# Performance work log

Hardware: AMD Instinct MI355X
Metric: run time of the kernel (lower is better)

Reference implementation:

```python
import jax, jax.numpy as jnp
import numpy as np

N_U = 8192  # users (rows of adj)
N_I = 8192  # items (cols of adj)
D_IN = 2048
D_H = 2048


def setup_inputs() -> dict:
    key = jax.random.key(0)
    k1, k2, k3, k4, k5 = jax.random.split(key, 5)
    input = jax.random.normal(k1, (N_U + N_I, D_IN), dtype=jnp.float32)
    adj = jax.random.uniform(k2, (N_U, N_I), dtype=jnp.float32)
    degree = jax.random.uniform(k3, (N_U + N_I,), dtype=jnp.float32)
    # Linear params (torch Linear: y = x @ W.T + b), xavier-normal-ish init
    W = jax.random.normal(k4, (D_H, D_IN), dtype=jnp.float32) * (2.0 / (D_IN + D_H)) ** 0.5
    b = jax.random.normal(k5, (D_H,), dtype=jnp.float32) * 0.01
    return {"input": input, "adj": adj, "degree": degree, "W": W, "b": b}


def reference(input, adj, degree, W, b):
    # Original builds block adjacency B = [[0, A], [A^T, 0]], then
    # output = diag(degree) @ B @ (dropout(input) @ W^T + b).
    # dropout p=0 (eval) -> identity. We avoid materializing B: the block
    # structure means user rows aggregate item supports and vice versa.
    n_u = adj.shape[0]
    support = input @ W.T + b                      # [N_u+N_i, D_h]
    sup_u, sup_i = support[:n_u], support[n_u:]
    out_u = degree[:n_u, None] * (adj @ sup_i)     # [N_u, D_h]
    out_i = degree[n_u:, None] * (adj.T @ sup_u)   # [N_i, D_h]
    return jnp.concatenate([out_u, out_i], axis=0)
```

## Files before the change

### kernel.cpp

```cpp
#include <hip/hip_runtime.h>
#include <hip/hip_bf16.h>


typedef __bf16 bf16;
typedef bf16 bf16x4 __attribute__((ext_vector_type(4)));
typedef bf16 bf16x8 __attribute__((ext_vector_type(8)));
typedef float f32x4 __attribute__((ext_vector_type(4)));

#define AS1 __attribute__((address_space(1)))
#define AS3 __attribute__((address_space(3)))

__global__ __launch_bounds__(256) void k_cvt(const float* __restrict__ src,
                                             bf16* __restrict__ dst) {
  long i = ((long)blockIdx.x * 256 + threadIdx.x) * 4;
  float4 v = *(const float4*)(src + i);
  bf16x4 o;
  o.x = (bf16)v.x; o.y = (bf16)v.y; o.z = (bf16)v.z; o.w = (bf16)v.w;
  *(bf16x4*)(dst + i) = o;
}

__global__ __launch_bounds__(256) void k_transpose_cvt(const float* __restrict__ src,
                                                       bf16* __restrict__ dst, int n) {
  __shared__ float tile[64][65];
  const int bx = blockIdx.x * 64;
  const int by = blockIdx.y * 64;
  const int tx = threadIdx.x & 15, ty = threadIdx.x >> 4;
#pragma unroll
  for (int p = 0; p < 4; ++p) {
    float4 v = *(const float4*)(src + (long)(by + p * 16 + ty) * n + bx + tx * 4);
    tile[p * 16 + ty][tx * 4 + 0] = v.x;
    tile[p * 16 + ty][tx * 4 + 1] = v.y;
    tile[p * 16 + ty][tx * 4 + 2] = v.z;
    tile[p * 16 + ty][tx * 4 + 3] = v.w;
  }
  __syncthreads();
#pragma unroll
  for (int p = 0; p < 4; ++p) {
    bf16x4 o;
    o.x = (bf16)tile[tx * 4 + 0][p * 16 + ty];
    o.y = (bf16)tile[tx * 4 + 1][p * 16 + ty];
    o.z = (bf16)tile[tx * 4 + 2][p * 16 + ty];
    o.w = (bf16)tile[tx * 4 + 3][p * 16 + ty];
    *(bf16x4*)(dst + (long)(bx + p * 16 + ty) * n + by + tx * 4) = o;
  }
}

template <bool OUT_BF16>
__global__ __launch_bounds__(256) void k_gemm_nt(
    const bf16* __restrict__ A, const bf16* __restrict__ B, void* __restrict__ Cout,
    int K, int lda, int ldb, int ldc,
    const float* __restrict__ rowscale, const float* __restrict__ rowbias) {
  constexpr int BK = 64;
  __shared__ __align__(16) bf16 As[128 * BK];
  __shared__ __align__(16) bf16 Bs[128 * BK];
  const int tid = threadIdx.x;
  const int wave = tid >> 6, lane = tid & 63;
  const int quad = lane >> 4, l16 = lane & 15;
  const int bm = blockIdx.y * 128, bn = blockIdx.x * 128;
  const bf16* Ab = A + (long)bm * lda;
  const bf16* Bb = B + (long)bn * ldb;
  f32x4 acc[4][4] = {};
  const int mrow = (wave & 1) * 64 + l16;
  const int ncol = (wave >> 1) * 64 + l16;
  const int xm = l16 & 7;

  for (int k0 = 0; k0 < K; k0 += BK) {
    __syncthreads();
#pragma unroll
    for (int it = 0; it < 4; ++it) {
      const int c = it * 256 + tid;
      const int row = c >> 3;
      const int kc = ((c & 7) ^ (row & 7)) * 8;
      __builtin_amdgcn_global_load_lds((AS1 void*)(Ab + row * lda + k0 + kc),
                                       (AS3 void*)(As + c * 8), 16, 0, 0);
      __builtin_amdgcn_global_load_lds((AS1 void*)(Bb + row * ldb + k0 + kc),
                                       (AS3 void*)(Bs + c * 8), 16, 0, 0);
    }
    __syncthreads();
#pragma unroll
    for (int ks = 0; ks < 2; ++ks) {
      const int jl = ks * 4 + quad;
      bf16x8 af[4], bfr[4];
#pragma unroll
      for (int i = 0; i < 4; ++i)
        af[i] = *(const bf16x8*)(As + (mrow + i * 16) * BK + ((jl ^ xm) << 3));
#pragma unroll
      for (int j = 0; j < 4; ++j)
        bfr[j] = *(const bf16x8*)(Bs + (ncol + j * 16) * BK + ((jl ^ xm) << 3));
#pragma unroll
      for (int i = 0; i < 4; ++i)
#pragma unroll
        for (int j = 0; j < 4; ++j)
          acc[i][j] = __builtin_amdgcn_mfma_f32_16x16x32_bf16(af[i], bfr[j], acc[i][j], 0, 0, 0);
    }
  }

#pragma unroll
  for (int i = 0; i < 4; ++i) {
    const int r0 = bm + (wave & 1) * 64 + i * 16 + quad * 4;
    float sc[4], bi[4];
#pragma unroll
    for (int r = 0; r < 4; ++r) {
      sc[r] = rowscale ? rowscale[r0 + r] : 1.0f;
      bi[r] = rowbias ? rowbias[r0 + r] : 0.0f;
    }
#pragma unroll
    for (int j = 0; j < 4; ++j) {
      const int col = bn + (wave >> 1) * 64 + j * 16 + l16;
#pragma unroll
      for (int r = 0; r < 4; ++r) {
        float v = acc[i][j][r] * sc[r] + bi[r];
        long idx = (long)(r0 + r) * ldc + col;
        if (OUT_BF16) ((bf16*)Cout)[idx] = (bf16)v;
        else          ((float*)Cout)[idx] = v;
      }
    }
  }
}

extern "C" void kernel_launch(void* const* d_in, const int* in_sizes, int n_in,
                              void* d_out, int out_size, void* d_ws, size_t ws_size,
                              hipStream_t stream) {
  const float* input  = (const float*)d_in[0];
  const float* adj    = (const float*)d_in[1];
  const float* degree = (const float*)d_in[2];
  const float* W      = (const float*)d_in[3];
  const float* b      = (const float*)d_in[4];
  float* out = (float*)d_out;

  char* ws = (char*)d_ws;
  bf16* supT   = (bf16*)(ws);
  bf16* in_bf  = (bf16*)(ws + (64ULL  << 20));
  bf16* W_bf   = (bf16*)(ws + (128ULL << 20));
  bf16* adj_bf = (bf16*)(ws + (64ULL  << 20));
  bf16* adjT   = (bf16*)(ws + (192ULL << 20));

  k_cvt<<<(16384 * 2048 / 4) / 256, 256, 0, stream>>>(input, in_bf);
  k_cvt<<<(2048 * 2048 / 4) / 256, 256, 0, stream>>>(W, W_bf);

  k_gemm_nt<true><<<dim3(16384 / 128, 2048 / 128), 256, 0, stream>>>(
      W_bf, in_bf, supT, 2048, 2048, 2048, 16384, nullptr, b);

  k_cvt<<<(8192 * 8192 / 4) / 256, 256, 0, stream>>>(adj, adj_bf);
  k_transpose_cvt<<<dim3(128, 128), 256, 0, stream>>>(adj, adjT, 8192);

  k_gemm_nt<false><<<dim3(2048 / 128, 8192 / 128), 256, 0, stream>>>(
      adj_bf, supT + 8192, out, 8192, 8192, 16384, 2048, degree, nullptr);

  k_gemm_nt<false><<<dim3(2048 / 128, 8192 / 128), 256, 0, stream>>>(
      adjT, supT, out + 8192LL * 2048, 8192, 8192, 16384, 2048, degree + 8192, nullptr);
}
```

Baseline: 1.423 ms.

## Fuse adj conversion passes, merge big GEMMs, add XCD-aware block swizzle

The separate adj bf16 cast and transpose-cast kernels become one kernel that reads adj once and writes both the row-major and transposed bf16 copies, which removes a full 256MB fp32 read. The two adjacency GEMMs are merged into a single launch using blockIdx.z, which removes a launch and tail gap. A block-index remap spreads contiguous row tiles across the 8 XCDs so tiles sharing A rows land on the same XCD's L2. The remap assumes grid.y is divisible by 8, and the merged kernel hard-codes the problem shapes.

New measurement: 1.458 ms. 1.02x slower.

```diff
diff --git a/kernel.cpp b/kernel.cpp
--- a/kernel.cpp
+++ b/kernel.cpp
@@ -19,15 +19,20 @@
   *(bf16x4*)(dst + i) = o;
 }
 
-__global__ __launch_bounds__(256) void k_transpose_cvt(const float* __restrict__ src,
-                                                       bf16* __restrict__ dst, int n) {
+__global__ __launch_bounds__(256) void k_adj_cvt_both(const float* __restrict__ src,
+                                                      bf16* __restrict__ dstS,
+                                                      bf16* __restrict__ dstT, int n) {
   __shared__ float tile[64][65];
   const int bx = blockIdx.x * 64;
   const int by = blockIdx.y * 64;
   const int tx = threadIdx.x & 15, ty = threadIdx.x >> 4;
 #pragma unroll
   for (int p = 0; p < 4; ++p) {
-    float4 v = *(const float4*)(src + (long)(by + p * 16 + ty) * n + bx + tx * 4);
+    const int row = by + p * 16 + ty;
+    float4 v = *(const float4*)(src + (long)row * n + bx + tx * 4);
+    bf16x4 s;
+    s.x = (bf16)v.x; s.y = (bf16)v.y; s.z = (bf16)v.z; s.w = (bf16)v.w;
+    *(bf16x4*)(dstS + (long)row * n + bx + tx * 4) = s;
     tile[p * 16 + ty][tx * 4 + 0] = v.x;
     tile[p * 16 + ty][tx * 4 + 1] = v.y;
     tile[p * 16 + ty][tx * 4 + 2] = v.z;
@@ -41,14 +46,22 @@
     o.y = (bf16)tile[tx * 4 + 1][p * 16 + ty];
     o.z = (bf16)tile[tx * 4 + 2][p * 16 + ty];
     o.w = (bf16)tile[tx * 4 + 3][p * 16 + ty];
-    *(bf16x4*)(dst + (long)(bx + p * 16 + ty) * n + by + tx * 4) = o;
+    *(bf16x4*)(dstT + (long)(bx + p * 16 + ty) * n + by + tx * 4) = o;
   }
 }
 
+__device__ inline void swizzle_xy(int nx, int ny, int& bxn, int& byn) {
+  const int id = blockIdx.y * nx + blockIdx.x;
+  const int xcd = id & 7;
+  const int slot = id >> 3;
+  bxn = slot % nx;
+  byn = xcd * (ny >> 3) + slot / nx;
+}
+
 template <bool OUT_BF16>
-__global__ __launch_bounds__(256) void k_gemm_nt(
+__device__ inline void gemm_nt_body(
     const bf16* __restrict__ A, const bf16* __restrict__ B, void* __restrict__ Cout,
-    int K, int lda, int ldb, int ldc,
+    int K, int lda, int ldb, int ldc, int bm, int bn,
     const float* __restrict__ rowscale, const float* __restrict__ rowbias) {
   constexpr int BK = 64;
   __shared__ __align__(16) bf16 As[128 * BK];
@@ -56,7 +69,6 @@
   const int tid = threadIdx.x;
   const int wave = tid >> 6, lane = tid & 63;
   const int quad = lane >> 4, l16 = lane & 15;
-  const int bm = blockIdx.y * 128, bn = blockIdx.x * 128;
   const bf16* Ab = A + (long)bm * lda;
   const bf16* Bb = B + (long)bn * ldb;
   f32x4 acc[4][4] = {};
@@ -118,6 +130,27 @@
   }
 }
 
+__global__ __launch_bounds__(256) void k_gemm_nt_bf16out(
+    const bf16* __restrict__ A, const bf16* __restrict__ B, bf16* __restrict__ C,
+    int K, int lda, int ldb, int ldc, const float* __restrict__ rowbias) {
+  int bxn, byn;
+  swizzle_xy((int)gridDim.x, (int)gridDim.y, bxn, byn);
+  gemm_nt_body<true>(A, B, C, K, lda, ldb, ldc, byn * 128, bxn * 128, nullptr, rowbias);
+}
+
+__global__ __launch_bounds__(256) void k_gemm_big(
+    const bf16* __restrict__ A0, const bf16* __restrict__ A1,
+    const bf16* __restrict__ B0, const bf16* __restrict__ B1,
+    float* __restrict__ out, const float* __restrict__ degree) {
+  int bxn, byn;
+  swizzle_xy((int)gridDim.x, (int)gridDim.y, bxn, byn);
+  const int z = blockIdx.z;
+  const bf16* A = z ? A1 : A0;
+  const bf16* B = z ? B1 : B0;
+  gemm_nt_body<false>(A, B, out + (long)z * 8192 * 2048, 8192, 8192, 16384, 2048,
+                      byn * 128, bxn * 128, degree + z * 8192, nullptr);
+}
+
 extern "C" void kernel_launch(void* const* d_in, const int* in_sizes, int n_in,
                               void* d_out, int out_size, void* d_ws, size_t ws_size,
                               hipStream_t stream) {
@@ -138,15 +171,11 @@
   k_cvt<<<(16384 * 2048 / 4) / 256, 256, 0, stream>>>(input, in_bf);
   k_cvt<<<(2048 * 2048 / 4) / 256, 256, 0, stream>>>(W, W_bf);
 
-  k_gemm_nt<true><<<dim3(16384 / 128, 2048 / 128), 256, 0, stream>>>(
-      W_bf, in_bf, supT, 2048, 2048, 2048, 16384, nullptr, b);
+  k_gemm_nt_bf16out<<<dim3(16384 / 128, 2048 / 128), 256, 0, stream>>>(
+      W_bf, in_bf, supT, 2048, 2048, 2048, 16384, b);
 
-  k_cvt<<<(8192 * 8192 / 4) / 256, 256, 0, stream>>>(adj, adj_bf);
-  k_transpose_cvt<<<dim3(128, 128), 256, 0, stream>>>(adj, adjT, 8192);
+  k_adj_cvt_both<<<dim3(128, 128), 256, 0, stream>>>(adj, adj_bf, adjT, 8192);
 
-  k_gemm_nt<false><<<dim3(2048 / 128, 8192 / 128), 256, 0, stream>>>(
-      adj_bf, supT + 8192, out, 8192, 8192, 16384, 2048, degree, nullptr);
-
-  k_gemm_nt<false><<<dim3(2048 / 128, 8192 / 128), 256, 0, stream>>>(
-      adjT, supT, out + 8192LL * 2048, 8192, 8192, 16384, 2048, degree + 8192, nullptr);
+  k_gemm_big<<<dim3(2048 / 128, 8192 / 128, 2), 256, 0, stream>>>(
+      adj_bf, adjT, supT + 8192, supT, out, degree);
 }
```
